# Performance work log

Measured on AMD Instinct MI355X. Metric: run time of the kernel, lower is better.

The kernel has to match this reference:

```python
import jax, jax.numpy as jnp
import numpy as np


def _cayley():
    # Cl(3,0) basis blades ordered by grade, lexicographic: 1,e1,e2,e3,e12,e13,e23,e123
    blades = [0b000, 0b001, 0b010, 0b100, 0b011, 0b101, 0b110, 0b111]
    idx = {b: i for i, b in enumerate(blades)}
    C = np.zeros((8, 8, 8), np.float32)
    for a in blades:
        for b in blades:
            t, s = a >> 1, 0
            while t:
                s += bin(t & b).count('1')
                t >>= 1
            C[idx[a], idx[a ^ b], idx[b]] = -1.0 if (s & 1) else 1.0
    return jnp.asarray(C)

CAYLEY = _cayley()                      # [8,8,8], metric [1,1,1]
GRADE = jnp.array([0, 1, 1, 1, 2, 2, 2, 3])  # blade -> grade (subspace) index
N_NODES, N_EDGES = 5, 20
NUM_HEADS = 8


def mv_linear(x, w, b):
    # MVLinear with subspaces=True: one scalar weight per (out, in, grade),
    # expanded to the 8 blades; bias only on the grade-0 (scalar) blade.
    # x: [N, m, 8], w: [n, m, 4], b: [n]
    out = jnp.einsum('bmi,nmi->bni', x, w[:, :, GRADE])
    return out.at[..., 0].add(b)


def _ln(x, g, b):
    m = jnp.mean(x, axis=-1, keepdims=True)
    v = jnp.var(x, axis=-1, keepdims=True)
    return (x - m) * jax.lax.rsqrt(v + 1e-5) * g + b


def _forward(nodes, edges, src_mask, batch_size, W_in, b_in, W_gp, b_gp,
             Wq, Wk, Wv, Wo, ln1_g, ln1_b, ln2_g, ln2_b, W1, b1, W2, b2):
    B = batch_size
    S = N_NODES + N_EDGES
    c_in = nodes.shape[1]
    nodes4 = nodes.reshape(B, N_NODES, c_in, 8)
    edges4 = edges.reshape(B, N_EDGES, c_in, 8)
    src = jnp.concatenate([nodes4, edges4], axis=1).reshape(B * S, c_in, 8)

    src_mv = mv_linear(src, W_in, b_in)                               # [B*S, dm, 8]
    src_gp = jnp.einsum('bni,ijk,bnk->bnj', src_mv, CAYLEY, src_mv)   # geometric product
    src2 = mv_linear(jnp.concatenate([src_mv, src_gp], axis=1), W_gp, b_gp)

    dm = src2.shape[1]
    D = dm * 8                                                        # 56 flat features
    H = NUM_HEADS
    hd = D // H
    x = src2.reshape(B, S, D)

    L = Wq.shape[0]
    for l in range(L):                                                # fixed small layer count
        h = _ln(x, ln1_g[l], ln1_b[l])
        q = (h @ Wq[l]).reshape(B, S, H, hd)
        k = (h @ Wk[l]).reshape(B, S, H, hd)
        v = (h @ Wv[l]).reshape(B, S, H, hd)
        scores = jnp.einsum('bqhd,bkhd->bhqk', q, k) / jnp.sqrt(jnp.float32(hd))
        scores = scores + src_mask[:, None, :, :]
        attn = jax.nn.softmax(scores, axis=-1)
        o = jnp.einsum('bhqk,bkhd->bqhd', attn, v).reshape(B, S, D)
        x = x + o @ Wo[l]
        h2 = _ln(x, ln2_g[l], ln2_b[l])
        x = x + jax.nn.gelu(h2 @ W1[l] + b1[l]) @ W2[l] + b2[l]

    out = x.reshape(B, S, dm, 8)
    sel = out[:, :N_NODES, 1, :]                                      # feature channel 1
    return sel.reshape(B * N_NODES, 8)


def setup_inputs() -> dict:
    key = jax.random.key(0)
    ks = jax.random.split(key, 12)
    B, c_in, dm, L = 4096, 3, 7, 4
    D = dm * 8
    Dff = 4 * D

    def r(k, shp, s=0.02):
        return jax.random.normal(k, shp, jnp.float32) * s

    return dict(
        nodes=jax.random.normal(ks[0], (B * N_NODES, c_in, 8), jnp.float32),
        edges=jax.random.normal(ks[1], (B * N_EDGES, c_in, 8), jnp.float32),
        src_mask=jnp.zeros((B, 25, 25), jnp.float32),
        batch_size=B,
        W_in=r(ks[2], (dm, c_in, 4), 1.0 / np.sqrt(c_in)),
        b_in=jnp.zeros((dm,), jnp.float32),
        W_gp=r(ks[3], (dm, 2 * dm, 4), 1.0 / np.sqrt(2 * dm)),
        b_gp=jnp.zeros((dm,), jnp.float32),
        Wq=r(ks[4], (L, D, D)), Wk=r(ks[5], (L, D, D)),
        Wv=r(ks[6], (L, D, D)), Wo=r(ks[7], (L, D, D)),
        ln1_g=jnp.ones((L, D), jnp.float32), ln1_b=jnp.zeros((L, D), jnp.float32),
        ln2_g=jnp.ones((L, D), jnp.float32), ln2_b=jnp.zeros((L, D), jnp.float32),
        W1=r(ks[8], (L, D, Dff)), b1=jnp.zeros((L, Dff), jnp.float32),
        W2=r(ks[9], (L, Dff, D)), b2=jnp.zeros((L, D), jnp.float32),
    )


def reference(nodes, edges, src_mask, batch_size, W_in, b_in, W_gp, b_gp,
              Wq, Wk, Wv, Wo, ln1_g, ln1_b, ln2_g, ln2_b, W1, b1, W2, b2):
    return _forward(nodes, edges, src_mask, batch_size, W_in, b_in, W_gp, b_gp,
                    Wq, Wk, Wv, Wo, ln1_g, ln1_b, ln2_g, ln2_b, W1, b1, W2, b2)
```

## Files before the change

kernel.cpp:

```cpp
#include <hip/hip_runtime.h>
#include <math.h>

#define NTH 256
#define XSTR 60
#define QHSTR 72
#define FSTR 232
#define LOG2E 1.4426950408889634f

typedef __attribute__((ext_vector_type(8))) short short8;
typedef __attribute__((ext_vector_type(4))) float f32x4;
typedef _Float16 half2_t __attribute__((ext_vector_type(2)));

__device__ __forceinline__ half2_t as_h2(unsigned int u) {
    return __builtin_bit_cast(half2_t, u);
}

__device__ __forceinline__ float fast_exp2(float x) {
    float r;
    asm("v_exp_f32 %0, %1" : "=v"(r) : "v"(x));
    return r;
}

__device__ __forceinline__ unsigned short f2bf(float x) {
    unsigned int u = __float_as_uint(x);
    return (unsigned short)((u + 0x7FFFu + ((u >> 16) & 1u)) >> 16);
}
__device__ __forceinline__ unsigned short f2bf_t(float x) {
    return (unsigned short)(__float_as_uint(x) >> 16);
}

__host__ __device__ constexpr int pc_(int v) { int c = 0; while (v) { c += v & 1; v >>= 1; } return c; }
__host__ __device__ constexpr int gp_sign(int a, int b) {
    int s = 0; int t = a >> 1;
    while (t) { s += pc_(t & b); t >>= 1; }
    return (s & 1) ? -1 : 1;
}
#define BLADE(i) ((int)((0x76534210u >> ((i) * 4)) & 0xF))

__device__ __forceinline__ float gelu_sig(float z) {
    float E = fast_exp2(-2.4554669f * z);
    return z * __builtin_amdgcn_rcpf(1.0f + E);
}

__global__ void prep_weights(const float* __restrict__ Wq, const float* __restrict__ Wk,
                             const float* __restrict__ Wv, const float* __restrict__ Wo,
                             const float* __restrict__ W1, const float* __restrict__ W2,
                             unsigned short* __restrict__ ws, int L)
{
    int idx = blockIdx.x * NTH + threadIdx.x;
    int total1 = L * 16384, total2 = L * 14336, total3 = L * 14336;
    if (idx < total1) {
        int k = idx & 63, n = (idx >> 6) & 63, mat = (idx >> 12) & 3, l = idx >> 14;
        float v = 0.f;
        if (k < 56 && n < 56) {
            const float* W = (mat == 0) ? Wq : (mat == 1) ? Wk : (mat == 2) ? Wv : Wo;
            v = W[l * 3136 + k * 56 + n];
            if (mat == 0) v *= 0.3779644730092272f * LOG2E;
        }
        ws[idx] = f2bf(v);
    } else if (idx < total1 + total2) {
        int t = idx - total1;
        int k = t & 63, n = (t >> 6) % 224, l = t / 14336;
        float v = (k < 56) ? W1[l * 12544 + k * 224 + n] : 0.f;
        ws[idx] = f2bf(v);
    } else if (idx < total1 + total2 + total3) {
        int t = idx - total1 - total2;
        int k = t % 224, n = (t / 224) & 63, l = t / 14336;
        float v = (n < 56) ? W2[l * 12544 + k * 56 + n] : 0.f;
        ws[idx] = f2bf(v);
    }
}

__global__ __launch_bounds__(NTH, 5) void nbody_fused(
    const float* __restrict__ nodes, const float* __restrict__ edges,
    const float* __restrict__ src_mask,
    const float* __restrict__ W_in, const float* __restrict__ b_in,
    const float* __restrict__ W_gp, const float* __restrict__ b_gp,
    const float* __restrict__ ln1g, const float* __restrict__ ln1b,
    const float* __restrict__ ln2g, const float* __restrict__ ln2b,
    const float* __restrict__ b1, const float* __restrict__ b2,
    const unsigned short* __restrict__ ws, int L,
    float* __restrict__ out)
{
    __shared__ __align__(16) float XS[25 * XSTR];
    __shared__ __align__(16) unsigned short HB[2304];
    __shared__ __align__(16) unsigned short UNI[5800];
    __shared__ __align__(16) float MKF[625];

    _Float16* QH = (_Float16*)UNI;
    _Float16* KH = QH + 25 * QHSTR;
    _Float16* VH = KH + 25 * QHSTR;
    unsigned short* FB = UNI;
    float* SRCF = XS;
    float* KBs = (float*)UNI;
    float* VBs = KBs + 25 * 57;

    const int b = blockIdx.x, tid = threadIdx.x;
    const int lane = tid & 63, wid = tid >> 6;
    const int nl = lane & 15, quad = lane >> 4;
    const int col = wid * 16 + nl;
    const int pcolh = (col / 7) * 8 + col % 7;
    const int ln_g = lane >> 3, ln_p = lane & 7;
    const int ln_s = wid + 4 * ln_g;

    for (int t = tid; t < 600; t += NTH) {
        int s = t / 24, r = t % 24;
        SRCF[t] = (s < 5) ? nodes[b * 120 + t] : edges[b * 480 + (s - 5) * 24 + r];
    }
    for (int t = tid; t < 625; t += NTH) MKF[t] = src_mask[b * 625 + t] * LOG2E;
    {
        int r = tid >> 3, c = 56 + (tid & 7);
        HB[r * 72 + c] = 0;
    }
    __syncthreads();

    for (int t = tid; t < 1400; t += NTH) {
        int s = t / 56, rem = t % 56, n = rem >> 3, i = rem & 7;
        int g = __popc(BLADE(i));
        float acc = (i == 0) ? b_in[n] : 0.0f;
        #pragma unroll
        for (int m = 0; m < 3; m++)
            acc += SRCF[s * 24 + m * 8 + i] * W_in[n * 12 + m * 4 + g];
        KBs[s * 57 + rem] = acc;
    }
    __syncthreads();

    for (int t = tid; t < 175; t += NTH) {
        int s = t / 7, n = t % 7;
        float m8[8], g8[8];
        #pragma unroll
        for (int i = 0; i < 8; i++) { m8[i] = KBs[s * 57 + n * 8 + i]; g8[i] = 0.0f; }
        #pragma unroll
        for (int ai = 0; ai < 8; ai++) {
            const int a = BLADE(ai);
            #pragma unroll
            for (int bi = 0; bi < 8; bi++) {
                const int bb = BLADE(bi);
                const int j = BLADE(a ^ bb);
                const int sg = gp_sign(a, bb);
                g8[j] += (sg > 0) ? (m8[ai] * m8[bi]) : (-m8[ai] * m8[bi]);
            }
        }
        #pragma unroll
        for (int j = 0; j < 8; j++) VBs[s * 57 + n * 8 + j] = g8[j];
    }
    __syncthreads();

    for (int t = tid; t < 1400; t += NTH) {
        int s = t / 56, rem = t % 56, n = rem >> 3, i = rem & 7;
        int g = __popc(BLADE(i));
        float acc = (i == 0) ? b_gp[n] : 0.0f;
        #pragma unroll
        for (int m = 0; m < 7; m++)
            acc += KBs[s * 57 + m * 8 + i] * W_gp[n * 56 + m * 4 + g];
        #pragma unroll
        for (int m = 0; m < 7; m++)
            acc += VBs[s * 57 + m * 8 + i] * W_gp[n * 56 + (7 + m) * 4 + g];
        XS[s * XSTR + rem] = acc;
    }
    __syncthreads();

    const unsigned short* w1t_all = ws + (size_t)L * 16384;
    const unsigned short* w2t_all = w1t_all + (size_t)L * 14336;

    for (int l = 0; l < L; l++) {
        const float* g1 = ln1g + l * 56; const float* e1 = ln1b + l * 56;
        const float* g2 = ln2g + l * 56; const float* e2 = ln2b + l * 56;

        if (tid < 200) {
            int s = tid >> 3, hh = tid & 7;
            QH[s * QHSTR + hh * 8 + 7] = (_Float16)0.f;
            KH[s * QHSTR + hh * 8 + 7] = (_Float16)0.f;
        }
        {
            float x[7]; float sum = 0.f, sq = 0.f;
            if (ln_s < 25) {
                const float* xp = XS + ln_s * XSTR + ln_p * 7;
                #pragma unroll
                for (int j = 0; j < 7; j++) { x[j] = xp[j]; sum += x[j]; sq += x[j] * x[j]; }
            }
            #pragma unroll
            for (int off = 1; off < 8; off <<= 1) {
                sum += __shfl_xor(sum, off, 64);
                sq  += __shfl_xor(sq,  off, 64);
            }
            if (ln_s < 25) {
                float mean = sum * (1.0f / 56.0f);
                float rs = __builtin_amdgcn_rsqf(sq * (1.0f / 56.0f) - mean * mean + 1e-5f);
                unsigned short* hp = HB + ln_s * 72 + ln_p * 7;
                #pragma unroll
                for (int j = 0; j < 7; j++) {
                    int d = ln_p * 7 + j;
                    hp[j] = f2bf_t((x[j] - mean) * rs * g1[d] + e1[d]);
                }
            }
        }
        __syncthreads();

        {
            short8 a[2][2];
            #pragma unroll
            for (int mt = 0; mt < 2; mt++)
                #pragma unroll
                for (int ks = 0; ks < 2; ks++)
                    a[mt][ks] = *(const short8*)(HB + (mt * 16 + nl) * 72 + ks * 32 + quad * 8);
            #pragma unroll
            for (int mat = 0; mat < 3; mat++) {
                const unsigned short* bp = ws + (((size_t)(l * 4 + mat)) << 12) + (((size_t)col) << 6) + quad * 8;
                short8 b0 = *(const short8*)(bp);
                short8 b1f = *(const short8*)(bp + 32);
                f32x4 acc0 = {0, 0, 0, 0}, acc1 = {0, 0, 0, 0};
                acc0 = __builtin_amdgcn_mfma_f32_16x16x32_bf16(a[0][0], b0, acc0, 0, 0, 0);
                acc0 = __builtin_amdgcn_mfma_f32_16x16x32_bf16(a[0][1], b1f, acc0, 0, 0, 0);
                acc1 = __builtin_amdgcn_mfma_f32_16x16x32_bf16(a[1][0], b0, acc1, 0, 0, 0);
                acc1 = __builtin_amdgcn_mfma_f32_16x16x32_bf16(a[1][1], b1f, acc1, 0, 0, 0);
                _Float16* dst = (mat == 0) ? QH : (mat == 1) ? KH : VH;
                if (col < 56) {
                    #pragma unroll
                    for (int r = 0; r < 4; r++) {
                        int row0 = quad * 4 + r;
                        dst[row0 * QHSTR + pcolh] = (_Float16)acc0[r];
                        int row1 = 16 + row0;
                        if (row1 < 25) dst[row1 * QHSTR + pcolh] = (_Float16)acc1[r];
                    }
                }
            }
        }
        __syncthreads();

        if (tid < 200) {
            int s = tid >> 3, hh = tid & 7;
            uint4 Q = *(const uint4*)(QH + s * QHSTR + hh * 8);
            half2_t q0 = as_h2(Q.x), q1 = as_h2(Q.y), q2 = as_h2(Q.z), q3 = as_h2(Q.w);
            float lsum = 0.f;
            half2_t acc0 = {0, 0}, acc1 = {0, 0}, acc2 = {0, 0}, acc3 = {0, 0};
            #pragma unroll 2
            for (int kk = 0; kk < 25; kk++) {
                uint4 K = *(const uint4*)(KH + kk * QHSTR + hh * 8);
                float dot = MKF[s * 25 + kk];
                dot = __builtin_amdgcn_fdot2(q3, as_h2(K.w), dot, false);
                dot = __builtin_amdgcn_fdot2(q2, as_h2(K.z), dot, false);
                dot = __builtin_amdgcn_fdot2(q1, as_h2(K.y), dot, false);
                dot = __builtin_amdgcn_fdot2(q0, as_h2(K.x), dot, false);
                float p = fast_exp2(dot);
                lsum += p;
                uint4 V = *(const uint4*)(VH + kk * QHSTR + hh * 8);
                _Float16 ph = (_Float16)p;
                half2_t p2 = {ph, ph};
                acc0 += p2 * as_h2(V.x); acc1 += p2 * as_h2(V.y);
                acc2 += p2 * as_h2(V.z); acc3 += p2 * as_h2(V.w);
            }
            float inv = __builtin_amdgcn_rcpf(lsum);
            unsigned short* op = HB + s * 72 + hh * 7;
            op[0] = f2bf_t((float)acc0.x * inv); op[1] = f2bf_t((float)acc0.y * inv);
            op[2] = f2bf_t((float)acc1.x * inv); op[3] = f2bf_t((float)acc1.y * inv);
            op[4] = f2bf_t((float)acc2.x * inv); op[5] = f2bf_t((float)acc2.y * inv);
            op[6] = f2bf_t((float)acc3.x * inv);
        }
        __syncthreads();

        {
            short8 a[2][2];
            #pragma unroll
            for (int mt = 0; mt < 2; mt++)
                #pragma unroll
                for (int ks = 0; ks < 2; ks++)
                    a[mt][ks] = *(const short8*)(HB + (mt * 16 + nl) * 72 + ks * 32 + quad * 8);
            const unsigned short* bp = ws + (((size_t)(l * 4 + 3)) << 12) + (((size_t)col) << 6) + quad * 8;
            short8 b0 = *(const short8*)(bp);
            short8 b1f = *(const short8*)(bp + 32);
            f32x4 acc0 = {0, 0, 0, 0}, acc1 = {0, 0, 0, 0};
            acc0 = __builtin_amdgcn_mfma_f32_16x16x32_bf16(a[0][0], b0, acc0, 0, 0, 0);
            acc0 = __builtin_amdgcn_mfma_f32_16x16x32_bf16(a[0][1], b1f, acc0, 0, 0, 0);
            acc1 = __builtin_amdgcn_mfma_f32_16x16x32_bf16(a[1][0], b0, acc1, 0, 0, 0);
            acc1 = __builtin_amdgcn_mfma_f32_16x16x32_bf16(a[1][1], b1f, acc1, 0, 0, 0);
            if (col < 56) {
                #pragma unroll
                for (int r = 0; r < 4; r++) {
                    int row0 = quad * 4 + r;
                    XS[row0 * XSTR + col] += acc0[r];
                    int row1 = 16 + row0;
                    if (row1 < 25) XS[row1 * XSTR + col] += acc1[r];
                }
            }
        }
        __syncthreads();

        {
            float x[7]; float sum = 0.f, sq = 0.f;
            if (ln_s < 25) {
                const float* xp = XS + ln_s * XSTR + ln_p * 7;
                #pragma unroll
                for (int j = 0; j < 7; j++) { x[j] = xp[j]; sum += x[j]; sq += x[j] * x[j]; }
            }
            #pragma unroll
            for (int off = 1; off < 8; off <<= 1) {
                sum += __shfl_xor(sum, off, 64);
                sq  += __shfl_xor(sq,  off, 64);
            }
            if (ln_s < 25) {
                float mean = sum * (1.0f / 56.0f);
                float rs = __builtin_amdgcn_rsqf(sq * (1.0f / 56.0f) - mean * mean + 1e-5f);
                unsigned short* hp = HB + ln_s * 72 + ln_p * 7;
                #pragma unroll
                for (int j = 0; j < 7; j++) {
                    int d = ln_p * 7 + j;
                    hp[j] = f2bf_t((x[j] - mean) * rs * g2[d] + e2[d]);
                }
            }
        }
        __syncthreads();

        {
            short8 a[2][2];
            #pragma unroll
            for (int mt = 0; mt < 2; mt++)
                #pragma unroll
                for (int ks = 0; ks < 2; ks++)
                    a[mt][ks] = *(const short8*)(HB + (mt * 16 + nl) * 72 + ks * 32 + quad * 8);
            for (int u = wid; u < 14; u += 4) {
                int c1 = u * 16 + nl;
                const unsigned short* bp = w1t_all + (((size_t)(l * 224 + c1)) << 6) + quad * 8;
                short8 b0 = *(const short8*)(bp);
                short8 b1f = *(const short8*)(bp + 32);
                f32x4 acc0 = {0, 0, 0, 0}, acc1 = {0, 0, 0, 0};
                acc0 = __builtin_amdgcn_mfma_f32_16x16x32_bf16(a[0][0], b0, acc0, 0, 0, 0);
                acc0 = __builtin_amdgcn_mfma_f32_16x16x32_bf16(a[0][1], b1f, acc0, 0, 0, 0);
                acc1 = __builtin_amdgcn_mfma_f32_16x16x32_bf16(a[1][0], b0, acc1, 0, 0, 0);
                acc1 = __builtin_amdgcn_mfma_f32_16x16x32_bf16(a[1][1], b1f, acc1, 0, 0, 0);
                float bias = b1[l * 224 + c1];
                #pragma unroll
                for (int r = 0; r < 4; r++) {
                    int row0 = quad * 4 + r;
                    FB[row0 * FSTR + c1] = f2bf_t(gelu_sig(acc0[r] + bias));
                    int row1 = 16 + row0;
                    if (row1 < 25) FB[row1 * FSTR + c1] = f2bf_t(gelu_sig(acc1[r] + bias));
                }
            }
        }
        __syncthreads();

        {
            int r1 = 16 + nl; if (r1 > 24) r1 = 24;
            const unsigned short* a0p = FB + nl * FSTR;
            const unsigned short* a1p = FB + r1 * FSTR;
            const unsigned short* bp0 = w2t_all + ((size_t)(l * 64 + col)) * 224 + quad * 8;
            f32x4 acc0 = {0, 0, 0, 0}, acc1 = {0, 0, 0, 0};
            #pragma unroll
            for (int ks = 0; ks < 7; ks++) {
                short8 bfrag = *(const short8*)(bp0 + ks * 32);
                short8 a0 = *(const short8*)(a0p + ks * 32 + quad * 8);
                short8 a1 = *(const short8*)(a1p + ks * 32 + quad * 8);
                acc0 = __builtin_amdgcn_mfma_f32_16x16x32_bf16(a0, bfrag, acc0, 0, 0, 0);
                acc1 = __builtin_amdgcn_mfma_f32_16x16x32_bf16(a1, bfrag, acc1, 0, 0, 0);
            }
            if (col < 56) {
                float bias = b2[l * 56 + col];
                #pragma unroll
                for (int r = 0; r < 4; r++) {
                    int row0 = quad * 4 + r;
                    XS[row0 * XSTR + col] += acc0[r] + bias;
                    int row1 = 16 + row0;
                    if (row1 < 25) XS[row1 * XSTR + col] += acc1[r] + bias;
                }
            }
        }
        __syncthreads();
    }

    for (int t = tid; t < 40; t += NTH) {
        int s = t >> 3, j = t & 7;
        out[(b * 5 + s) * 8 + j] = XS[s * XSTR + 8 + j];
    }
}

extern "C" void kernel_launch(void* const* d_in, const int* in_sizes, int n_in,
                              void* d_out, int out_size, void* d_ws, size_t ws_size,
                              hipStream_t stream) {
    const float* nodes = (const float*)d_in[0];
    const float* edges = (const float*)d_in[1];
    const float* mask  = (const float*)d_in[2];
    const int B = in_sizes[0] / 120;
    const float* W_in = (const float*)d_in[4];
    const float* b_in = (const float*)d_in[5];
    const float* W_gp = (const float*)d_in[6];
    const float* b_gp = (const float*)d_in[7];
    const float* Wq   = (const float*)d_in[8];
    const float* Wk   = (const float*)d_in[9];
    const float* Wv   = (const float*)d_in[10];
    const float* Wo   = (const float*)d_in[11];
    const float* ln1g = (const float*)d_in[12];
    const float* ln1b = (const float*)d_in[13];
    const float* ln2g = (const float*)d_in[14];
    const float* ln2b = (const float*)d_in[15];
    const float* W1   = (const float*)d_in[16];
    const float* b1   = (const float*)d_in[17];
    const float* W2   = (const float*)d_in[18];
    const float* b2   = (const float*)d_in[19];
    float* out = (float*)d_out;
    const int L = in_sizes[8] / 3136;

    unsigned short* ws16 = (unsigned short*)d_ws;
    int prep_total = L * (16384 + 14336 + 14336);
    hipLaunchKernelGGL(prep_weights, dim3((prep_total + NTH - 1) / NTH), dim3(NTH), 0, stream,
                       Wq, Wk, Wv, Wo, W1, W2, ws16, L);

    hipLaunchKernelGGL(nbody_fused, dim3(B), dim3(NTH), 0, stream,
                       nodes, edges, mask, W_in, b_in, W_gp, b_gp,
                       ln1g, ln1b, ln2g, ln2b, b1, b2, ws16, L, out);
}
```

Before: 310.8 us.

## Process two batch samples per 512-thread block, pooling attention threads across both

Each block now runs 512 threads and handles two batch elements, with each 256-thread half owning its own shared-memory buffers. The attention phase lets 400 threads cover both samples' 200 (row, head) tasks, so fewer threads sit idle there. The aim is to halve the block count and amortise per-block setup and barriers over two samples. In exchange, shared memory and register pressure per block double, occupancy hints drop from 5 to 4 blocks per CU, and every barrier now spans both halves.

```diff
diff --git a/kernel.cpp b/kernel.cpp
--- a/kernel.cpp
+++ b/kernel.cpp
@@ -1,7 +1,8 @@
 #include <hip/hip_runtime.h>
 #include <math.h>
 
-#define NTH 256
+#define NTH 512
+#define PTH 256
 #define XSTR 60
 #define QHSTR 72
 #define FSTR 232
@@ -14,13 +15,11 @@
 __device__ __forceinline__ half2_t as_h2(unsigned int u) {
     return __builtin_bit_cast(half2_t, u);
 }
-
 __device__ __forceinline__ float fast_exp2(float x) {
     float r;
     asm("v_exp_f32 %0, %1" : "=v"(r) : "v"(x));
     return r;
 }
-
 __device__ __forceinline__ unsigned short f2bf(float x) {
     unsigned int u = __float_as_uint(x);
     return (unsigned short)((u + 0x7FFFu + ((u >> 16) & 1u)) >> 16);
@@ -47,7 +46,7 @@
                              const float* __restrict__ W1, const float* __restrict__ W2,
                              unsigned short* __restrict__ ws, int L)
 {
-    int idx = blockIdx.x * NTH + threadIdx.x;
+    int idx = blockIdx.x * PTH + threadIdx.x;
     int total1 = L * 16384, total2 = L * 14336, total3 = L * 14336;
     if (idx < total1) {
         int k = idx & 63, n = (idx >> 6) & 63, mat = (idx >> 12) & 3, l = idx >> 14;
@@ -71,7 +70,7 @@
     }
 }
 
-__global__ __launch_bounds__(NTH, 5) void nbody_fused(
+__global__ __launch_bounds__(NTH, 4) void nbody_fused(
     const float* __restrict__ nodes, const float* __restrict__ edges,
     const float* __restrict__ src_mask,
     const float* __restrict__ W_in, const float* __restrict__ b_in,
@@ -79,84 +78,101 @@
     const float* __restrict__ ln1g, const float* __restrict__ ln1b,
     const float* __restrict__ ln2g, const float* __restrict__ ln2b,
     const float* __restrict__ b1, const float* __restrict__ b2,
-    const unsigned short* __restrict__ ws, int L,
+    const unsigned short* __restrict__ ws, int L, int Btot,
     float* __restrict__ out)
 {
-    __shared__ __align__(16) float XS[25 * XSTR];
-    __shared__ __align__(16) unsigned short HB[2304];
-    __shared__ __align__(16) unsigned short UNI[5800];
-    __shared__ __align__(16) float MKF[625];
-
-    _Float16* QH = (_Float16*)UNI;
-    _Float16* KH = QH + 25 * QHSTR;
-    _Float16* VH = KH + 25 * QHSTR;
-    unsigned short* FB = UNI;
-    float* SRCF = XS;
-    float* KBs = (float*)UNI;
-    float* VBs = KBs + 25 * 57;
-
-    const int b = blockIdx.x, tid = threadIdx.x;
-    const int lane = tid & 63, wid = tid >> 6;
+    __shared__ __align__(16) float XS[2][25 * XSTR];
+    __shared__ __align__(16) unsigned short HB[2][2304];
+    __shared__ __align__(16) unsigned short UNI[2][5800];
+    __shared__ __align__(16) float MKF[2][625];
+
+    const int tid = threadIdx.x;
+    const int ss = tid >> 8;
+    const int t = tid & 255;
+    const int lane = t & 63, wid = t >> 6;
     const int nl = lane & 15, quad = lane >> 4;
     const int col = wid * 16 + nl;
     const int pcolh = (col / 7) * 8 + col % 7;
     const int ln_g = lane >> 3, ln_p = lane & 7;
     const int ln_s = wid + 4 * ln_g;
-
-    for (int t = tid; t < 600; t += NTH) {
-        int s = t / 24, r = t % 24;
-        SRCF[t] = (s < 5) ? nodes[b * 120 + t] : edges[b * 480 + (s - 5) * 24 + r];
-    }
-    for (int t = tid; t < 625; t += NTH) MKF[t] = src_mask[b * 625 + t] * LOG2E;
+    const int b0 = blockIdx.x * 2;
+    const int bb = b0 + ss;
+    const bool valid = (bb < Btot);
+
+    _Float16* QH = (_Float16*)UNI[ss];
+    _Float16* KH = QH + 25 * QHSTR;
+    _Float16* VH = KH + 25 * QHSTR;
+    unsigned short* FB = UNI[ss];
+    float* XSs = XS[ss];
+    unsigned short* HBs = HB[ss];
+
+    if (valid) {
+        for (int i = t; i < 600; i += PTH) {
+            int s = i / 24, r = i % 24;
+            XSs[i] = (s < 5) ? nodes[bb * 120 + i] : edges[bb * 480 + (s - 5) * 24 + r];
+        }
+        for (int i = t; i < 625; i += PTH) MKF[ss][i] = src_mask[bb * 625 + i] * LOG2E;
+    }
     {
-        int r = tid >> 3, c = 56 + (tid & 7);
-        HB[r * 72 + c] = 0;
+        int r = t >> 3, c = 56 + (t & 7);
+        HBs[r * 72 + c] = 0;
     }
     __syncthreads();
 
-    for (int t = tid; t < 1400; t += NTH) {
-        int s = t / 56, rem = t % 56, n = rem >> 3, i = rem & 7;
-        int g = __popc(BLADE(i));
-        float acc = (i == 0) ? b_in[n] : 0.0f;
-        #pragma unroll
-        for (int m = 0; m < 3; m++)
-            acc += SRCF[s * 24 + m * 8 + i] * W_in[n * 12 + m * 4 + g];
-        KBs[s * 57 + rem] = acc;
+    {
+        float* KBs = (float*)UNI[ss];
+        for (int i = t; i < 1400; i += PTH) {
+            int s = i / 56, rem = i % 56, n = rem >> 3, ii = rem & 7;
+            int g = __popc(BLADE(ii));
+            float acc = (ii == 0) ? b_in[n] : 0.0f;
+            #pragma unroll
+            for (int m = 0; m < 3; m++)
+                acc += XSs[s * 24 + m * 8 + ii] * W_in[n * 12 + m * 4 + g];
+            KBs[s * 57 + rem] = acc;
+        }
     }
     __syncthreads();
 
-    for (int t = tid; t < 175; t += NTH) {
-        int s = t / 7, n = t % 7;
-        float m8[8], g8[8];
-        #pragma unroll
-        for (int i = 0; i < 8; i++) { m8[i] = KBs[s * 57 + n * 8 + i]; g8[i] = 0.0f; }
-        #pragma unroll
-        for (int ai = 0; ai < 8; ai++) {
-            const int a = BLADE(ai);
-            #pragma unroll
-            for (int bi = 0; bi < 8; bi++) {
-                const int bb = BLADE(bi);
-                const int j = BLADE(a ^ bb);
-                const int sg = gp_sign(a, bb);
-                g8[j] += (sg > 0) ? (m8[ai] * m8[bi]) : (-m8[ai] * m8[bi]);
-            }
-        }
-        #pragma unroll
-        for (int j = 0; j < 8; j++) VBs[s * 57 + n * 8 + j] = g8[j];
+    {
+        float* KBs = (float*)UNI[ss];
+        float* VBs = KBs + 25 * 57;
+        for (int i = t; i < 175; i += PTH) {
+            int s = i / 7, n = i % 7;
+            float m8[8], g8[8];
+            #pragma unroll
+            for (int j = 0; j < 8; j++) { m8[j] = KBs[s * 57 + n * 8 + j]; g8[j] = 0.0f; }
+            #pragma unroll
+            for (int ai = 0; ai < 8; ai++) {
+                const int a = BLADE(ai);
+                #pragma unroll
+                for (int bi = 0; bi < 8; bi++) {
+                    const int bbb = BLADE(bi);
+                    const int j = BLADE(a ^ bbb);
+                    const int sg = gp_sign(a, bbb);
+                    g8[j] += (sg > 0) ? (m8[ai] * m8[bi]) : (-m8[ai] * m8[bi]);
+                }
+            }
+            #pragma unroll
+            for (int j = 0; j < 8; j++) VBs[s * 57 + n * 8 + j] = g8[j];
+        }
     }
     __syncthreads();
 
-    for (int t = tid; t < 1400; t += NTH) {
-        int s = t / 56, rem = t % 56, n = rem >> 3, i = rem & 7;
-        int g = __popc(BLADE(i));
-        float acc = (i == 0) ? b_gp[n] : 0.0f;
-        #pragma unroll
-        for (int m = 0; m < 7; m++)
-            acc += KBs[s * 57 + m * 8 + i] * W_gp[n * 56 + m * 4 + g];
-        #pragma unroll
-        for (int m = 0; m < 7; m++)
-            acc += VBs[s * 57 + m * 8 + i] * W_gp[n * 56 + (7 + m) * 4 + g];
-        XS[s * XSTR + rem] = acc;
+    {
+        const float* KBs = (const float*)UNI[ss];
+        const float* VBs = KBs + 25 * 57;
+        for (int i = t; i < 1400; i += PTH) {
+            int s = i / 56, rem = i % 56, n = rem >> 3, ii = rem & 7;
+            int g = __popc(BLADE(ii));
+            float acc = (ii == 0) ? b_gp[n] : 0.0f;
+            #pragma unroll
+            for (int m = 0; m < 7; m++)
+                acc += KBs[s * 57 + m * 8 + ii] * W_gp[n * 56 + m * 4 + g];
+            #pragma unroll
+            for (int m = 0; m < 7; m++)
+                acc += VBs[s * 57 + m * 8 + ii] * W_gp[n * 56 + (7 + m) * 4 + g];
+            XSs[s * XSTR + rem] = acc;
+        }
     }
     __syncthreads();
 
@@ -167,15 +183,15 @@
         const float* g1 = ln1g + l * 56; const float* e1 = ln1b + l * 56;
         const float* g2 = ln2g + l * 56; const float* e2 = ln2b + l * 56;
 
-        if (tid < 200) {
-            int s = tid >> 3, hh = tid & 7;
+        if (t < 200) {
+            int s = t >> 3, hh = t & 7;
             QH[s * QHSTR + hh * 8 + 7] = (_Float16)0.f;
             KH[s * QHSTR + hh * 8 + 7] = (_Float16)0.f;
         }
         {
             float x[7]; float sum = 0.f, sq = 0.f;
             if (ln_s < 25) {
-                const float* xp = XS + ln_s * XSTR + ln_p * 7;
+                const float* xp = XSs + ln_s * XSTR + ln_p * 7;
                 #pragma unroll
                 for (int j = 0; j < 7; j++) { x[j] = xp[j]; sum += x[j]; sq += x[j] * x[j]; }
             }
@@ -187,7 +203,7 @@
             if (ln_s < 25) {
                 float mean = sum * (1.0f / 56.0f);
                 float rs = __builtin_amdgcn_rsqf(sq * (1.0f / 56.0f) - mean * mean + 1e-5f);
-                unsigned short* hp = HB + ln_s * 72 + ln_p * 7;
+                unsigned short* hp = HBs + ln_s * 72 + ln_p * 7;
                 #pragma unroll
                 for (int j = 0; j < 7; j++) {
                     int d = ln_p * 7 + j;
@@ -203,18 +219,18 @@
             for (int mt = 0; mt < 2; mt++)
                 #pragma unroll
                 for (int ks = 0; ks < 2; ks++)
-                    a[mt][ks] = *(const short8*)(HB + (mt * 16 + nl) * 72 + ks * 32 + quad * 8);
+                    a[mt][ks] = *(const short8*)(HBs + (mt * 16 + nl) * 72 + ks * 32 + quad * 8);
             #pragma unroll
             for (int mat = 0; mat < 3; mat++) {
                 const unsigned short* bp = ws + (((size_t)(l * 4 + mat)) << 12) + (((size_t)col) << 6) + quad * 8;
-                short8 b0 = *(const short8*)(bp);
+                short8 b0f = *(const short8*)(bp);
                 short8 b1f = *(const short8*)(bp + 32);
                 f32x4 acc0 = {0, 0, 0, 0}, acc1 = {0, 0, 0, 0};
-                acc0 = __builtin_amdgcn_mfma_f32_16x16x32_bf16(a[0][0], b0, acc0, 0, 0, 0);
+                acc0 = __builtin_amdgcn_mfma_f32_16x16x32_bf16(a[0][0], b0f, acc0, 0, 0, 0);
                 acc0 = __builtin_amdgcn_mfma_f32_16x16x32_bf16(a[0][1], b1f, acc0, 0, 0, 0);
-                acc1 = __builtin_amdgcn_mfma_f32_16x16x32_bf16(a[1][0], b0, acc1, 0, 0, 0);
+                acc1 = __builtin_amdgcn_mfma_f32_16x16x32_bf16(a[1][0], b0f, acc1, 0, 0, 0);
                 acc1 = __builtin_amdgcn_mfma_f32_16x16x32_bf16(a[1][1], b1f, acc1, 0, 0, 0);
-                _Float16* dst = (mat == 0) ? QH : (mat == 1) ? KH : VH;
+                _Float16* dst = QH + mat * 25 * QHSTR;
                 if (col < 56) {
                     #pragma unroll
                     for (int r = 0; r < 4; r++) {
@@ -228,30 +244,35 @@
         }
         __syncthreads();
 
-        if (tid < 200) {
-            int s = tid >> 3, hh = tid & 7;
-            uint4 Q = *(const uint4*)(QH + s * QHSTR + hh * 8);
+        if (tid < 400) {
+            int ss2 = tid / 200;
+            int r = tid - ss2 * 200;
+            int s = r >> 3, hh = r & 7;
+            const _Float16* QH2 = (const _Float16*)UNI[ss2];
+            const _Float16* KH2 = QH2 + 25 * QHSTR;
+            const _Float16* VH2 = KH2 + 25 * QHSTR;
+            uint4 Q = *(const uint4*)(QH2 + s * QHSTR + hh * 8);
             half2_t q0 = as_h2(Q.x), q1 = as_h2(Q.y), q2 = as_h2(Q.z), q3 = as_h2(Q.w);
             float lsum = 0.f;
             half2_t acc0 = {0, 0}, acc1 = {0, 0}, acc2 = {0, 0}, acc3 = {0, 0};
             #pragma unroll 2
             for (int kk = 0; kk < 25; kk++) {
-                uint4 K = *(const uint4*)(KH + kk * QHSTR + hh * 8);
-                float dot = MKF[s * 25 + kk];
+                uint4 K = *(const uint4*)(KH2 + kk * QHSTR + hh * 8);
+                float dot = MKF[ss2][s * 25 + kk];
                 dot = __builtin_amdgcn_fdot2(q3, as_h2(K.w), dot, false);
                 dot = __builtin_amdgcn_fdot2(q2, as_h2(K.z), dot, false);
                 dot = __builtin_amdgcn_fdot2(q1, as_h2(K.y), dot, false);
                 dot = __builtin_amdgcn_fdot2(q0, as_h2(K.x), dot, false);
                 float p = fast_exp2(dot);
                 lsum += p;
-                uint4 V = *(const uint4*)(VH + kk * QHSTR + hh * 8);
+                uint4 V = *(const uint4*)(VH2 + kk * QHSTR + hh * 8);
                 _Float16 ph = (_Float16)p;
                 half2_t p2 = {ph, ph};
                 acc0 += p2 * as_h2(V.x); acc1 += p2 * as_h2(V.y);
                 acc2 += p2 * as_h2(V.z); acc3 += p2 * as_h2(V.w);
             }
             float inv = __builtin_amdgcn_rcpf(lsum);
-            unsigned short* op = HB + s * 72 + hh * 7;
+            unsigned short* op = HB[ss2] + s * 72 + hh * 7;
             op[0] = f2bf_t((float)acc0.x * inv); op[1] = f2bf_t((float)acc0.y * inv);
             op[2] = f2bf_t((float)acc1.x * inv); op[3] = f2bf_t((float)acc1.y * inv);
             op[4] = f2bf_t((float)acc2.x * inv); op[5] = f2bf_t((float)acc2.y * inv);
@@ -265,22 +286,22 @@
             for (int mt = 0; mt < 2; mt++)
                 #pragma unroll
                 for (int ks = 0; ks < 2; ks++)
-                    a[mt][ks] = *(const short8*)(HB + (mt * 16 + nl) * 72 + ks * 32 + quad * 8);
+                    a[mt][ks] = *(const short8*)(HBs + (mt * 16 + nl) * 72 + ks * 32 + quad * 8);
             const unsigned short* bp = ws + (((size_t)(l * 4 + 3)) << 12) + (((size_t)col) << 6) + quad * 8;
-            short8 b0 = *(const short8*)(bp);
+            short8 b0f = *(const short8*)(bp);
             short8 b1f = *(const short8*)(bp + 32);
             f32x4 acc0 = {0, 0, 0, 0}, acc1 = {0, 0, 0, 0};
-            acc0 = __builtin_amdgcn_mfma_f32_16x16x32_bf16(a[0][0], b0, acc0, 0, 0, 0);
+            acc0 = __builtin_amdgcn_mfma_f32_16x16x32_bf16(a[0][0], b0f, acc0, 0, 0, 0);
             acc0 = __builtin_amdgcn_mfma_f32_16x16x32_bf16(a[0][1], b1f, acc0, 0, 0, 0);
-            acc1 = __builtin_amdgcn_mfma_f32_16x16x32_bf16(a[1][0], b0, acc1, 0, 0, 0);
+            acc1 = __builtin_amdgcn_mfma_f32_16x16x32_bf16(a[1][0], b0f, acc1, 0, 0, 0);
             acc1 = __builtin_amdgcn_mfma_f32_16x16x32_bf16(a[1][1], b1f, acc1, 0, 0, 0);
             if (col < 56) {
                 #pragma unroll
                 for (int r = 0; r < 4; r++) {
                     int row0 = quad * 4 + r;
-                    XS[row0 * XSTR + col] += acc0[r];
+                    XSs[row0 * XSTR + col] += acc0[r];
                     int row1 = 16 + row0;
-                    if (row1 < 25) XS[row1 * XSTR + col] += acc1[r];
+                    if (row1 < 25) XSs[row1 * XSTR + col] += acc1[r];
                 }
             }
         }
@@ -289,7 +310,7 @@
         {
             float x[7]; float sum = 0.f, sq = 0.f;
             if (ln_s < 25) {
-                const float* xp = XS + ln_s * XSTR + ln_p * 7;
+                const float* xp = XSs + ln_s * XSTR + ln_p * 7;
                 #pragma unroll
                 for (int j = 0; j < 7; j++) { x[j] = xp[j]; sum += x[j]; sq += x[j] * x[j]; }
             }
@@ -301,7 +322,7 @@
             if (ln_s < 25) {
                 float mean = sum * (1.0f / 56.0f);
                 float rs = __builtin_amdgcn_rsqf(sq * (1.0f / 56.0f) - mean * mean + 1e-5f);
-                unsigned short* hp = HB + ln_s * 72 + ln_p * 7;
+                unsigned short* hp = HBs + ln_s * 72 + ln_p * 7;
                 #pragma unroll
                 for (int j = 0; j < 7; j++) {
                     int d = ln_p * 7 + j;
@@ -317,16 +338,16 @@
             for (int mt = 0; mt < 2; mt++)
                 #pragma unroll
                 for (int ks = 0; ks < 2; ks++)
-                    a[mt][ks] = *(const short8*)(HB + (mt * 16 + nl) * 72 + ks * 32 + quad * 8);
+                    a[mt][ks] = *(const short8*)(HBs + (mt * 16 + nl) * 72 + ks * 32 + quad * 8);
             for (int u = wid; u < 14; u += 4) {
                 int c1 = u * 16 + nl;
                 const unsigned short* bp = w1t_all + (((size_t)(l * 224 + c1)) << 6) + quad * 8;
-                short8 b0 = *(const short8*)(bp);
+                short8 b0f = *(const short8*)(bp);
                 short8 b1f = *(const short8*)(bp + 32);
                 f32x4 acc0 = {0, 0, 0, 0}, acc1 = {0, 0, 0, 0};
-                acc0 = __builtin_amdgcn_mfma_f32_16x16x32_bf16(a[0][0], b0, acc0, 0, 0, 0);
+                acc0 = __builtin_amdgcn_mfma_f32_16x16x32_bf16(a[0][0], b0f, acc0, 0, 0, 0);
                 acc0 = __builtin_amdgcn_mfma_f32_16x16x32_bf16(a[0][1], b1f, acc0, 0, 0, 0);
-                acc1 = __builtin_amdgcn_mfma_f32_16x16x32_bf16(a[1][0], b0, acc1, 0, 0, 0);
+                acc1 = __builtin_amdgcn_mfma_f32_16x16x32_bf16(a[1][0], b0f, acc1, 0, 0, 0);
                 acc1 = __builtin_amdgcn_mfma_f32_16x16x32_bf16(a[1][1], b1f, acc1, 0, 0, 0);
                 float bias = b1[l * 224 + c1];
                 #pragma unroll
@@ -359,18 +380,20 @@
                 #pragma unroll
                 for (int r = 0; r < 4; r++) {
                     int row0 = quad * 4 + r;
-                    XS[row0 * XSTR + col] += acc0[r] + bias;
+                    XSs[row0 * XSTR + col] += acc0[r] + bias;
                     int row1 = 16 + row0;
-                    if (row1 < 25) XS[row1 * XSTR + col] += acc1[r] + bias;
-                }
-            }
-        }
-        __syncthreads();
-    }
-
-    for (int t = tid; t < 40; t += NTH) {
-        int s = t >> 3, j = t & 7;
-        out[(b * 5 + s) * 8 + j] = XS[s * XSTR + 8 + j];
+                    if (row1 < 25) XSs[row1 * XSTR + col] += acc1[r] + bias;
+                }
+            }
+        }
+        __syncthreads();
+    }
+
+    if (valid) {
+        for (int i = t; i < 40; i += PTH) {
+            int s = i >> 3, j = i & 7;
+            out[(bb * 5 + s) * 8 + j] = XSs[s * XSTR + 8 + j];
+        }
     }
 }
 
@@ -402,10 +425,10 @@
 
     unsigned short* ws16 = (unsigned short*)d_ws;
     int prep_total = L * (16384 + 14336 + 14336);
-    hipLaunchKernelGGL(prep_weights, dim3((prep_total + NTH - 1) / NTH), dim3(NTH), 0, stream,
+    hipLaunchKernelGGL(prep_weights, dim3((prep_total + PTH - 1) / PTH), dim3(PTH), 0, stream,
                        Wq, Wk, Wv, Wo, W1, W2, ws16, L);
 
-    hipLaunchKernelGGL(nbody_fused, dim3(B), dim3(NTH), 0, stream,
+    hipLaunchKernelGGL(nbody_fused, dim3((B + 1) / 2), dim3(NTH), 0, stream,
                        nodes, edges, mask, W_in, b_in, W_gp, b_gp,
-                       ln1g, ln1b, ln2g, ln2b, b1, b2, ws16, L, out);
-}
+                       ln1g, ln1b, ln2g, ln2b, b1, b2, ws16, L, B, out);
+}
```

Result: slower. 340.8 us (+9.7%).
